# Optimization experiments

Measured on AMD Instinct MI355X. Metric: run time of the kernel, lower is better.

Reference implementation:

```python
import jax, jax.numpy as jnp
import numpy as np

EPS = 1e-5
N_LANG = 5

def _ln(x, gamma, beta):
    mu = jnp.mean(x, axis=-1, keepdims=True)
    var = jnp.mean((x - mu) ** 2, axis=-1, keepdims=True)
    return (x - mu) * jax.lax.rsqrt(var + EPS) * gamma + beta

def setup_inputs() -> dict:
    key = jax.random.key(0)
    ks = jax.random.split(key, 20)
    B, S, E, T, H = 16, 512, 768, 768, 1024
    s = lambda fan_in: 1.0 / np.sqrt(fan_in)
    inp = {
        'ner_features': jax.random.normal(ks[0], (B, S, E), jnp.float32),
        'topic_features': jax.random.normal(ks[1], (B, S, T), jnp.float32),
        'language_ids': jax.random.randint(ks[2], (B,), 0, N_LANG, jnp.int64),
        # ner transform: Linear(E,H) + LayerNorm(H)
        'W_ner': jax.random.uniform(ks[3], (E, H), jnp.float32, -s(E), s(E)),
        'b_ner': jnp.zeros((H,), jnp.float32),
        'g_ner': jnp.ones((H,), jnp.float32),
        'be_ner': jnp.zeros((H,), jnp.float32),
        # topic transform: Linear(T,H) + LayerNorm(H)
        'W_top': jax.random.uniform(ks[4], (T, H), jnp.float32, -s(T), s(T)),
        'b_top': jnp.zeros((H,), jnp.float32),
        'g_top': jnp.ones((H,), jnp.float32),
        'be_top': jnp.zeros((H,), jnp.float32),
        # 5 language gate networks, stacked on leading lang axis
        'Wg1': jax.random.uniform(ks[5], (N_LANG, 2 * H, H), jnp.float32, -s(2 * H), s(2 * H)),
        'bg1': jnp.zeros((N_LANG, H), jnp.float32),
        'gg': jnp.ones((N_LANG, H), jnp.float32),
        'bg': jnp.zeros((N_LANG, H), jnp.float32),
        'Wg2': jax.random.uniform(ks[6], (N_LANG, H, 2), jnp.float32, -s(H), s(H)),
        'bg2': jnp.zeros((N_LANG, 2), jnp.float32),
    }
    return inp

def reference(ner_features, topic_features, language_ids,
              W_ner, b_ner, g_ner, be_ner,
              W_top, b_top, g_top, be_top,
              Wg1, bg1, gg, bg, Wg2, bg2):
    # shared transforms: [B,S,H]
    ner_t = jax.nn.relu(_ln(ner_features @ W_ner + b_ner, g_ner, be_ner))
    top_t = jax.nn.relu(_ln(topic_features @ W_top + b_top, g_top, be_top))
    combined = jnp.concatenate([ner_t, top_t], axis=-1)  # [B,S,2H]
    # all-language gate MLPs (faithful to the original redundant compute)
    h = jnp.einsum('bsd,ldh->lbsh', combined, Wg1) + bg1[:, None, None, :]
    h = jax.nn.relu(_ln(h, gg[:, None, None, :], bg[:, None, None, :]))
    gates_all = jax.nn.sigmoid(jnp.einsum('lbsh,lhk->lbsk', h, Wg2) + bg2[:, None, None, :])  # [L,B,S,2]
    mask = (language_ids[None, :] == jnp.arange(N_LANG)[:, None]).astype(gates_all.dtype)  # [L,B]
    gates = jnp.einsum('lb,lbsk->bsk', mask, gates_all)  # [B,S,2]
    gated_ner = ner_t * gates[..., 0:1]
    gated_topic = top_t * gates[..., 1:2]
    # dropout in eval mode (identity) for determinism
    return gated_ner, gated_topic
```

## Files before the change

kernel.cpp:

```cpp
#include <hip/hip_runtime.h>

typedef __attribute__((ext_vector_type(8))) short short8;
typedef __attribute__((ext_vector_type(4))) float f32x4;

__device__ __forceinline__ float bf2f(unsigned short u) {
    union { unsigned int i; float f; } v; v.i = ((unsigned int)u) << 16; return v.f;
}
__device__ __forceinline__ unsigned short f2bf(float f) {
    union { float f; unsigned int i; } v; v.f = f;
    unsigned int r = v.i + 0x7fffu + ((v.i >> 16) & 1u);
    return (unsigned short)(r >> 16);
}
__device__ __forceinline__ void gload16(const unsigned short* g, unsigned short* l) {
    __builtin_amdgcn_global_load_lds(
        (const __attribute__((address_space(1))) unsigned int*)g,
        (__attribute__((address_space(3))) unsigned int*)l, 16, 0, 0);
}
__device__ __forceinline__ short8 cvt8(float4 a, float4 b) {
    short8 s;
    s[0] = (short)f2bf(a.x); s[1] = (short)f2bf(a.y);
    s[2] = (short)f2bf(a.z); s[3] = (short)f2bf(a.w);
    s[4] = (short)f2bf(b.x); s[5] = (short)f2bf(b.y);
    s[6] = (short)f2bf(b.z); s[7] = (short)f2bf(b.w);
    return s;
}

#define VM(n) asm volatile("s_waitcnt vmcnt(%0)" :: "i"(n) : "memory")
#define LGK0() asm volatile("s_waitcnt lgkmcnt(0)" ::: "memory")
#define SBAR() __builtin_amdgcn_s_barrier()
#define SCHED0() __builtin_amdgcn_sched_barrier(0)

__global__ __launch_bounds__(512, 4) void gemm_f32a(
    const float* __restrict__ nerA, const float* __restrict__ topA,
    const unsigned short* __restrict__ Bta,
    const unsigned short* __restrict__ Btb,
    const float* __restrict__ biasa,
    const float* __restrict__ biasb,
    unsigned short* __restrict__ Cb)
{
    constexpr int K = 768;
    constexpr int NT = K / 64;
    __shared__ __align__(16) unsigned short As0[128][64], Bs0[128][64];
    __shared__ __align__(16) unsigned short As1[128][64], Bs1[128][64];

    const int t = threadIdx.x;
    const int nx = gridDim.x;
    const int bid = blockIdx.y * nx + blockIdx.x;
    const int cpx = (nx * gridDim.y) >> 3;
    const int swz = (bid & 7) * cpx + (bid >> 3);
    const int gm0 = (swz >> 3) * 128;
    const int gn0 = (swz & 7) * 128;

    const int sel = gm0 >> 13;
    const unsigned short* Bt = sel ? Btb : Bta;
    const float* bias = sel ? biasb : biasa;
    const float* Ab = sel ? topA : nerA;

    const int lane = t & 63;
    const int w = t >> 6;
    const int wm = w >> 2, wn = w & 3;
    const int fr = lane & 15, g4 = lane >> 4, f7 = lane & 7;
    const int csw0 = ((0 + g4) ^ f7) * 8;
    const int csw1 = ((4 + g4) ^ f7) * 8;

    const int srow = t >> 3;
    const int swcol = ((t & 7) ^ (srow & 7)) * 8;
    const int lcol = (t & 7) * 8;
    const float* af = Ab + (size_t)((gm0 & 8191) + srow) * K + swcol;
    const unsigned short* bg = Bt + (size_t)(gn0 + srow) * K + swcol;

    f32x4 acc[4][2];
#pragma unroll
    for (int m = 0; m < 4; ++m)
#pragma unroll
        for (int n = 0; n < 2; ++n)
            acc[m][n] = (f32x4){0.f, 0.f, 0.f, 0.f};

    float4 rg0[4], rg1[4];

    auto issueA = [&](float4* rg, int k0) {
        const float4* p0 = (const float4*)(af + k0);
        const float4* p1 = (const float4*)(af + (size_t)64 * K + k0);
        rg[0] = p0[0]; rg[1] = p0[1];
        rg[2] = p1[0]; rg[3] = p1[1];
    };
    auto writeA = [&](unsigned short (*As)[64], const float4* rg) {
        *(short8*)&As[srow][lcol]      = cvt8(rg[0], rg[1]);
        *(short8*)&As[64 + srow][lcol] = cvt8(rg[2], rg[3]);
    };
    auto gloadB = [&](unsigned short (*Bs)[64], int k0) {
#pragma unroll
        for (int i = 0; i < 2; ++i)
            gload16(bg + (size_t)(i * 64) * K + k0, &Bs[i * 64 + srow][lcol]);
    };
    auto compute = [&](const unsigned short (*As)[64], const unsigned short (*Bs)[64]) {
        short8 a0[4], b0[2];
#pragma unroll
        for (int m = 0; m < 4; ++m) a0[m] = *(const short8*)&As[wm * 64 + m * 16 + fr][csw0];
#pragma unroll
        for (int n = 0; n < 2; ++n) b0[n] = *(const short8*)&Bs[wn * 32 + n * 16 + fr][csw0];
        __builtin_amdgcn_s_setprio(1);
#pragma unroll
        for (int m = 0; m < 4; ++m)
#pragma unroll
            for (int n = 0; n < 2; ++n)
                acc[m][n] = __builtin_amdgcn_mfma_f32_16x16x32_bf16(a0[m], b0[n], acc[m][n], 0, 0, 0);
        __builtin_amdgcn_s_setprio(0);
#pragma unroll
        for (int m = 0; m < 4; ++m) a0[m] = *(const short8*)&As[wm * 64 + m * 16 + fr][csw1];
#pragma unroll
        for (int n = 0; n < 2; ++n) b0[n] = *(const short8*)&Bs[wn * 32 + n * 16 + fr][csw1];
        __builtin_amdgcn_s_setprio(1);
#pragma unroll
        for (int m = 0; m < 4; ++m)
#pragma unroll
            for (int n = 0; n < 2; ++n)
                acc[m][n] = __builtin_amdgcn_mfma_f32_16x16x32_bf16(a0[m], b0[n], acc[m][n], 0, 0, 0);
        __builtin_amdgcn_s_setprio(0);
    };

    issueA(rg0, 0);
    gloadB(Bs0, 0);
    issueA(rg1, 64);
    gloadB(Bs1, 64);
    VM(8);
    writeA(As0, rg0);

    for (int tt = 0; tt < NT; tt += 2) {
        if (tt + 1 < NT) VM(2); else VM(0);
        if (tt + 1 < NT) writeA(As1, rg1);
        if (tt + 2 < NT) issueA(rg0, (tt + 2) * 64);
        LGK0();
        SBAR();
        SCHED0();
        compute(As0, Bs0);
        SCHED0();
        SBAR();
        if (tt + 2 < NT) gloadB(Bs0, (tt + 2) * 64);
        if (tt + 2 < NT) VM(2); else VM(0);
        if (tt + 2 < NT) writeA(As0, rg0);
        if (tt + 3 < NT) issueA(rg1, (tt + 3) * 64);
        LGK0();
        SBAR();
        SCHED0();
        compute(As1, Bs1);
        SCHED0();
        SBAR();
        if (tt + 3 < NT) gloadB(Bs1, (tt + 3) * 64);
    }

    const int fq = lane >> 4;
    const int rbase = gm0 & 8191;
    const size_t coloff = (size_t)sel * 1024;
#pragma unroll
    for (int n = 0; n < 2; ++n) {
        const int col = gn0 + wn * 32 + n * 16 + fr;
        const float bv = bias[col];
#pragma unroll
        for (int m = 0; m < 4; ++m) {
            const int row0 = rbase + wm * 64 + m * 16 + fq * 4;
#pragma unroll
            for (int r = 0; r < 4; ++r)
                Cb[(size_t)(row0 + r) * 2048 + coloff + col] = f2bf(acc[m][n][r] + bv);
        }
    }
}

__global__ __launch_bounds__(512, 4) void gemm_w8(
    const unsigned short* __restrict__ A,
    const unsigned short* __restrict__ Bta,
    const float* __restrict__ biasa,
    unsigned short* __restrict__ Cb,
    const int* __restrict__ lang)
{
    constexpr int K = 2048;
    __shared__ __align__(16) unsigned short As0[128][64], Bs0[128][64];
    __shared__ __align__(16) unsigned short As1[128][64], Bs1[128][64];

    const int t = threadIdx.x;
    const int nx = gridDim.x;
    const int bid = blockIdx.y * nx + blockIdx.x;
    const int cpx = (nx * gridDim.y) >> 3;
    const int swz = (bid & 7) * cpx + (bid >> 3);
    const int gm0 = (swz >> 3) * 128;
    const int gn0 = (swz & 7) * 128;

    const int l = lang[gm0 >> 9];
    const unsigned short* Bt = Bta + (size_t)l * ((size_t)K * 1024);
    const float* bias = biasa + l * 1024;

    const int lane = t & 63;
    const int w = t >> 6;
    const int wm = w >> 2, wn = w & 3;
    const int fr = lane & 15, g4 = lane >> 4, f7 = lane & 7;
    const int csw0 = ((0 + g4) ^ f7) * 8;
    const int csw1 = ((4 + g4) ^ f7) * 8;

    const int srow = t >> 3;
    const int swcol = ((t & 7) ^ (srow & 7)) * 8;
    const int lcol = (t & 7) * 8;
    const unsigned short* ag = A  + (size_t)(gm0 + srow) * K + swcol;
    const unsigned short* bg = Bt + (size_t)(gn0 + srow) * K + swcol;

    f32x4 acc[4][2];
#pragma unroll
    for (int m = 0; m < 4; ++m)
#pragma unroll
        for (int n = 0; n < 2; ++n)
            acc[m][n] = (f32x4){0.f, 0.f, 0.f, 0.f};

    auto stage = [&](unsigned short (*As)[64], unsigned short (*Bs)[64], int k0) {
#pragma unroll
        for (int i = 0; i < 2; ++i) {
            gload16(ag + (size_t)(i * 64) * K + k0, &As[i * 64 + srow][lcol]);
            gload16(bg + (size_t)(i * 64) * K + k0, &Bs[i * 64 + srow][lcol]);
        }
    };
    auto compute = [&](const unsigned short (*As)[64], const unsigned short (*Bs)[64]) {
        short8 a0[4], b0[2];
#pragma unroll
        for (int m = 0; m < 4; ++m) a0[m] = *(const short8*)&As[wm * 64 + m * 16 + fr][csw0];
#pragma unroll
        for (int n = 0; n < 2; ++n) b0[n] = *(const short8*)&Bs[wn * 32 + n * 16 + fr][csw0];
        __builtin_amdgcn_s_setprio(1);
#pragma unroll
        for (int m = 0; m < 4; ++m)
#pragma unroll
            for (int n = 0; n < 2; ++n)
                acc[m][n] = __builtin_amdgcn_mfma_f32_16x16x32_bf16(a0[m], b0[n], acc[m][n], 0, 0, 0);
        __builtin_amdgcn_s_setprio(0);
#pragma unroll
        for (int m = 0; m < 4; ++m) a0[m] = *(const short8*)&As[wm * 64 + m * 16 + fr][csw1];
#pragma unroll
        for (int n = 0; n < 2; ++n) b0[n] = *(const short8*)&Bs[wn * 32 + n * 16 + fr][csw1];
        __builtin_amdgcn_s_setprio(1);
#pragma unroll
        for (int m = 0; m < 4; ++m)
#pragma unroll
            for (int n = 0; n < 2; ++n)
                acc[m][n] = __builtin_amdgcn_mfma_f32_16x16x32_bf16(a0[m], b0[n], acc[m][n], 0, 0, 0);
        __builtin_amdgcn_s_setprio(0);
    };

    constexpr int NT = K / 64;
    stage(As0, Bs0, 0);
    stage(As1, Bs1, 64);

    for (int tt = 0; tt < NT; tt += 2) {
        VM(4);
        SBAR();
        asm volatile("" ::: "memory");
        SCHED0();
        compute(As0, Bs0);
        SCHED0();
        SBAR();
        if (tt + 2 < NT) stage(As0, Bs0, (tt + 2) * 64);
        if (tt + 2 < NT) VM(4); else VM(0);
        SBAR();
        asm volatile("" ::: "memory");
        SCHED0();
        compute(As1, Bs1);
        SCHED0();
        SBAR();
        if (tt + 3 < NT) stage(As1, Bs1, (tt + 3) * 64);
    }

    const int fq = lane >> 4;
#pragma unroll
    for (int n = 0; n < 2; ++n) {
        const int col = gn0 + wn * 32 + n * 16 + fr;
        const float bv = bias[col];
#pragma unroll
        for (int m = 0; m < 4; ++m) {
            const int row0 = gm0 + wm * 64 + m * 16 + fq * 4;
#pragma unroll
            for (int r = 0; r < 4; ++r)
                Cb[(size_t)(row0 + r) * 1024 + col] = f2bf(acc[m][n][r] + bv);
        }
    }
}

__device__ __forceinline__ void wt_tile(
    const float* W, unsigned short* Wt, int K, int N, int bx, int by,
    float (*tile)[33], int t)
{
    const int n0 = bx * 32, k0 = by * 32;
    const int x = t & 31, y = t >> 5;
#pragma unroll
    for (int i = 0; i < 4; ++i)
        tile[y + 8 * i][x] = W[(size_t)(k0 + y + 8 * i) * N + n0 + x];
    __syncthreads();
#pragma unroll
    for (int i = 0; i < 4; ++i)
        Wt[(size_t)(n0 + y + 8 * i) * K + k0 + x] = f2bf(tile[x][y + 8 * i]);
}

__global__ __launch_bounds__(256) void prep_all(
    const float* __restrict__ W_ner, unsigned short* __restrict__ W_nert,
    const float* __restrict__ W_top, unsigned short* __restrict__ W_topt,
    const float* __restrict__ Wg1,   unsigned short* __restrict__ Wg1t)
{
    __shared__ float tile[32][33];
    int b = blockIdx.x;
    const int t = threadIdx.x;
    if (b < 768)  { wt_tile(W_ner, W_nert, 768, 1024, b % 32, b / 32, tile, t); return; }
    b -= 768;
    if (b < 768)  { wt_tile(W_top, W_topt, 768, 1024, b % 32, b / 32, tile, t); return; }
    b -= 768;
    const int z = b / 2048, r = b % 2048;
    wt_tile(Wg1 + (size_t)z * 2097152, Wg1t + (size_t)z * 2097152,
            2048, 1024, r % 32, r / 32, tile, t);
}

__global__ __launch_bounds__(256) void ln_relu_c(
    unsigned short* __restrict__ comb,
    const float* __restrict__ gn, const float* __restrict__ bn,
    const float* __restrict__ gt, const float* __restrict__ btp)
{
    const int b = blockIdx.x, t = threadIdx.x;
    const int r = b >> 1, half = b & 1;
    unsigned short* p = comb + (size_t)r * 2048 + half * 1024 + t * 4;
    ushort4 u = *(const ushort4*)p;
    const float x0 = bf2f(u.x), x1 = bf2f(u.y), x2 = bf2f(u.z), x3 = bf2f(u.w);
    float s1 = x0 + x1 + x2 + x3;
    float s2 = x0 * x0 + x1 * x1 + x2 * x2 + x3 * x3;
#pragma unroll
    for (int off = 32; off > 0; off >>= 1) {
        s1 += __shfl_down(s1, off);
        s2 += __shfl_down(s2, off);
    }
    __shared__ float red[8];
    const int wid = t >> 6;
    if ((t & 63) == 0) { red[wid] = s1; red[4 + wid] = s2; }
    __syncthreads();
    s1 = red[0] + red[1] + red[2] + red[3];
    s2 = red[4] + red[5] + red[6] + red[7];
    const float mean = s1 * (1.0f / 1024.0f);
    const float var = fmaxf(s2 * (1.0f / 1024.0f) - mean * mean, 0.0f);
    const float rstd = rsqrtf(var + 1e-5f);
    const float* G  = half ? gt : gn;
    const float* Be = half ? btp : bn;
    const float4 g  = ((const float4*)G)[t];
    const float4 be = ((const float4*)Be)[t];
    u.x = f2bf(fmaxf((x0 - mean) * rstd * g.x + be.x, 0.0f));
    u.y = f2bf(fmaxf((x1 - mean) * rstd * g.y + be.y, 0.0f));
    u.z = f2bf(fmaxf((x2 - mean) * rstd * g.z + be.z, 0.0f));
    u.w = f2bf(fmaxf((x3 - mean) * rstd * g.w + be.w, 0.0f));
    *(ushort4*)p = u;
}

__global__ __launch_bounds__(256) void ln_gate(
    const unsigned short* __restrict__ preln, const unsigned short* __restrict__ comb,
    const float* __restrict__ gg, const float* __restrict__ bgb,
    const float* __restrict__ Wg2, const float* __restrict__ bg2,
    const int* __restrict__ lang,
    float* __restrict__ outN, float* __restrict__ outT)
{
    const int r = blockIdx.x, t = threadIdx.x;
    const int l = lang[r >> 9];
    const ushort4 u = *(const ushort4*)(preln + (size_t)r * 1024 + t * 4);
    const float x0 = bf2f(u.x), x1 = bf2f(u.y), x2 = bf2f(u.z), x3 = bf2f(u.w);
    float s1 = x0 + x1 + x2 + x3;
    float s2 = x0 * x0 + x1 * x1 + x2 * x2 + x3 * x3;
#pragma unroll
    for (int off = 32; off > 0; off >>= 1) {
        s1 += __shfl_down(s1, off);
        s2 += __shfl_down(s2, off);
    }
    __shared__ float red[8];
    const int wid = t >> 6;
    if ((t & 63) == 0) { red[wid] = s1; red[4 + wid] = s2; }
    __syncthreads();
    s1 = red[0] + red[1] + red[2] + red[3];
    s2 = red[4] + red[5] + red[6] + red[7];
    const float mean = s1 * (1.0f / 1024.0f);
    const float var = fmaxf(s2 * (1.0f / 1024.0f) - mean * mean, 0.0f);
    const float rstd = rsqrtf(var + 1e-5f);
    const float4 g  = ((const float4*)(gg + l * 1024))[t];
    const float4 be = ((const float4*)(bgb + l * 1024))[t];
    const float h0 = fmaxf((x0 - mean) * rstd * g.x + be.x, 0.0f);
    const float h1 = fmaxf((x1 - mean) * rstd * g.y + be.y, 0.0f);
    const float h2 = fmaxf((x2 - mean) * rstd * g.z + be.z, 0.0f);
    const float h3 = fmaxf((x3 - mean) * rstd * g.w + be.w, 0.0f);
    const float4* W = (const float4*)(Wg2 + (size_t)l * 2048);
    const float4 wa = W[t * 2], wb = W[t * 2 + 1];
    float d0 = h0 * wa.x + h1 * wa.z + h2 * wb.x + h3 * wb.z;
    float d1 = h0 * wa.y + h1 * wa.w + h2 * wb.y + h3 * wb.w;
#pragma unroll
    for (int off = 32; off > 0; off >>= 1) {
        d0 += __shfl_down(d0, off);
        d1 += __shfl_down(d1, off);
    }
    __syncthreads();
    if ((t & 63) == 0) { red[wid] = d0; red[4 + wid] = d1; }
    __syncthreads();
    d0 = red[0] + red[1] + red[2] + red[3] + bg2[l * 2 + 0];
    d1 = red[4] + red[5] + red[6] + red[7] + bg2[l * 2 + 1];
    const float g0 = 1.0f / (1.0f + __expf(-d0));
    const float g1 = 1.0f / (1.0f + __expf(-d1));
    const ushort4 cn = *(const ushort4*)(comb + (size_t)r * 2048 + t * 4);
    const ushort4 ct = *(const ushort4*)(comb + (size_t)r * 2048 + 1024 + t * 4);
    float4 a, b;
    a.x = bf2f(cn.x) * g0; a.y = bf2f(cn.y) * g0; a.z = bf2f(cn.z) * g0; a.w = bf2f(cn.w) * g0;
    b.x = bf2f(ct.x) * g1; b.y = bf2f(ct.y) * g1; b.z = bf2f(ct.z) * g1; b.w = bf2f(ct.w) * g1;
    ((float4*)(outN + (size_t)r * 1024))[t] = a;
    ((float4*)(outT + (size_t)r * 1024))[t] = b;
}

extern "C" void kernel_launch(void* const* d_in, const int* in_sizes, int n_in,
                              void* d_out, int out_size, void* d_ws, size_t ws_size,
                              hipStream_t stream)
{
    const float* ner    = (const float*)d_in[0];
    const float* top    = (const float*)d_in[1];
    const int*   lang   = (const int*)d_in[2];
    const float* W_ner  = (const float*)d_in[3];
    const float* b_ner  = (const float*)d_in[4];
    const float* g_ner  = (const float*)d_in[5];
    const float* be_ner = (const float*)d_in[6];
    const float* W_top  = (const float*)d_in[7];
    const float* b_top  = (const float*)d_in[8];
    const float* g_top  = (const float*)d_in[9];
    const float* be_top = (const float*)d_in[10];
    const float* Wg1    = (const float*)d_in[11];
    const float* bg1    = (const float*)d_in[12];
    const float* gg     = (const float*)d_in[13];
    const float* bgb    = (const float*)d_in[14];
    const float* Wg2    = (const float*)d_in[15];
    const float* bg2    = (const float*)d_in[16];

    float* out  = (float*)d_out;
    float* outN = out;
    float* outT = out + 8388608;

    char* ws = (char*)d_ws;
    unsigned short* combined = (unsigned short*)ws;
    unsigned short* preln2   = (unsigned short*)(ws + 33554432);
    unsigned short* Wg1t     = (unsigned short*)(ws + 58720256);
    unsigned short* W_nert   = (unsigned short*)outT;
    unsigned short* W_topt   = W_nert + 786432;

    prep_all<<<11776, 256, 0, stream>>>(W_ner, W_nert, W_top, W_topt, Wg1, Wg1t);

    gemm_f32a<<<dim3(8, 128), 512, 0, stream>>>(
        ner, top, W_nert, W_topt, b_ner, b_top, combined);
    ln_relu_c<<<16384, 256, 0, stream>>>(combined, g_ner, be_ner, g_top, be_top);

    gemm_w8<<<dim3(8, 64), 512, 0, stream>>>(combined, Wg1t, bg1, preln2, lang);

    ln_gate<<<8192, 256, 0, stream>>>(preln2, combined, gg, bgb, Wg2, bg2, lang, outN, outT);
}
```

Measured before the change: 138.6 us.

## Pre-convert activations to bf16 and use direct-to-LDS loads with BK=32 in first GEMM

The fp32 ner/topic activations are now converted to bf16 in the prep kernel and stored in workspace. The first GEMM then loads both A and B straight into LDS with global_load_lds, dropping the register staging and in-loop conversion. K-tile depth is halved to 32 to shrink LDS use, and the occupancy hint is raised to 8. The cost is an extra full read and write pass over the activations in the prep kernel, plus twice as many barrier-separated K iterations.

```diff
diff --git a/kernel.cpp b/kernel.cpp
--- a/kernel.cpp
+++ b/kernel.cpp
@@ -16,22 +16,13 @@
         (const __attribute__((address_space(1))) unsigned int*)g,
         (__attribute__((address_space(3))) unsigned int*)l, 16, 0, 0);
 }
-__device__ __forceinline__ short8 cvt8(float4 a, float4 b) {
-    short8 s;
-    s[0] = (short)f2bf(a.x); s[1] = (short)f2bf(a.y);
-    s[2] = (short)f2bf(a.z); s[3] = (short)f2bf(a.w);
-    s[4] = (short)f2bf(b.x); s[5] = (short)f2bf(b.y);
-    s[6] = (short)f2bf(b.z); s[7] = (short)f2bf(b.w);
-    return s;
-}
 
 #define VM(n) asm volatile("s_waitcnt vmcnt(%0)" :: "i"(n) : "memory")
-#define LGK0() asm volatile("s_waitcnt lgkmcnt(0)" ::: "memory")
 #define SBAR() __builtin_amdgcn_s_barrier()
 #define SCHED0() __builtin_amdgcn_sched_barrier(0)
 
-__global__ __launch_bounds__(512, 4) void gemm_f32a(
-    const float* __restrict__ nerA, const float* __restrict__ topA,
+__global__ __launch_bounds__(512, 8) void gemm1_bk32(
+    const unsigned short* __restrict__ A,
     const unsigned short* __restrict__ Bta,
     const unsigned short* __restrict__ Btb,
     const float* __restrict__ biasa,
@@ -39,9 +30,9 @@
     unsigned short* __restrict__ Cb)
 {
     constexpr int K = 768;
-    constexpr int NT = K / 64;
-    __shared__ __align__(16) unsigned short As0[128][64], Bs0[128][64];
-    __shared__ __align__(16) unsigned short As1[128][64], Bs1[128][64];
+    constexpr int NT = K / 32;
+    __shared__ __align__(16) unsigned short As0[128][32], Bs0[128][32];
+    __shared__ __align__(16) unsigned short As1[128][32], Bs1[128][32];
 
     const int t = threadIdx.x;
     const int nx = gridDim.x;
@@ -54,20 +45,17 @@
     const int sel = gm0 >> 13;
     const unsigned short* Bt = sel ? Btb : Bta;
     const float* bias = sel ? biasb : biasa;
-    const float* Ab = sel ? topA : nerA;
 
     const int lane = t & 63;
     const int w = t >> 6;
     const int wm = w >> 2, wn = w & 3;
-    const int fr = lane & 15, g4 = lane >> 4, f7 = lane & 7;
-    const int csw0 = ((0 + g4) ^ f7) * 8;
-    const int csw1 = ((4 + g4) ^ f7) * 8;
-
-    const int srow = t >> 3;
-    const int swcol = ((t & 7) ^ (srow & 7)) * 8;
-    const int lcol = (t & 7) * 8;
-    const float* af = Ab + (size_t)((gm0 & 8191) + srow) * K + swcol;
-    const unsigned short* bg = Bt + (size_t)(gn0 + srow) * K + swcol;
+    const int fr = lane & 15, g4 = lane >> 4;
+    const int csw = (g4 ^ ((fr >> 1) & 3)) * 8;
+
+    const int r = t >> 2, s = t & 3;
+    const int gc = (s ^ ((r >> 1) & 3)) * 8;
+    const unsigned short* ag = A  + (size_t)(gm0 + r) * K + gc;
+    const unsigned short* bg = Bt + (size_t)(gn0 + r) * K + gc;
 
     f32x4 acc[4][2];
 #pragma unroll
@@ -76,40 +64,16 @@
         for (int n = 0; n < 2; ++n)
             acc[m][n] = (f32x4){0.f, 0.f, 0.f, 0.f};
 
-    float4 rg0[4], rg1[4];
-
-    auto issueA = [&](float4* rg, int k0) {
-        const float4* p0 = (const float4*)(af + k0);
-        const float4* p1 = (const float4*)(af + (size_t)64 * K + k0);
-        rg[0] = p0[0]; rg[1] = p0[1];
-        rg[2] = p1[0]; rg[3] = p1[1];
+    auto stage = [&](unsigned short (*As)[32], unsigned short (*Bs)[32], int k0) {
+        gload16(ag + k0, &As[r][s * 8]);
+        gload16(bg + k0, &Bs[r][s * 8]);
     };
-    auto writeA = [&](unsigned short (*As)[64], const float4* rg) {
-        *(short8*)&As[srow][lcol]      = cvt8(rg[0], rg[1]);
-        *(short8*)&As[64 + srow][lcol] = cvt8(rg[2], rg[3]);
-    };
-    auto gloadB = [&](unsigned short (*Bs)[64], int k0) {
-#pragma unroll
-        for (int i = 0; i < 2; ++i)
-            gload16(bg + (size_t)(i * 64) * K + k0, &Bs[i * 64 + srow][lcol]);
-    };
-    auto compute = [&](const unsigned short (*As)[64], const unsigned short (*Bs)[64]) {
+    auto compute = [&](const unsigned short (*As)[32], const unsigned short (*Bs)[32]) {
         short8 a0[4], b0[2];
 #pragma unroll
-        for (int m = 0; m < 4; ++m) a0[m] = *(const short8*)&As[wm * 64 + m * 16 + fr][csw0];
-#pragma unroll
-        for (int n = 0; n < 2; ++n) b0[n] = *(const short8*)&Bs[wn * 32 + n * 16 + fr][csw0];
-        __builtin_amdgcn_s_setprio(1);
-#pragma unroll
-        for (int m = 0; m < 4; ++m)
-#pragma unroll
-            for (int n = 0; n < 2; ++n)
-                acc[m][n] = __builtin_amdgcn_mfma_f32_16x16x32_bf16(a0[m], b0[n], acc[m][n], 0, 0, 0);
-        __builtin_amdgcn_s_setprio(0);
-#pragma unroll
-        for (int m = 0; m < 4; ++m) a0[m] = *(const short8*)&As[wm * 64 + m * 16 + fr][csw1];
-#pragma unroll
-        for (int n = 0; n < 2; ++n) b0[n] = *(const short8*)&Bs[wn * 32 + n * 16 + fr][csw1];
+        for (int m = 0; m < 4; ++m) a0[m] = *(const short8*)&As[wm * 64 + m * 16 + fr][csw];
+#pragma unroll
+        for (int n = 0; n < 2; ++n) b0[n] = *(const short8*)&Bs[wn * 32 + n * 16 + fr][csw];
         __builtin_amdgcn_s_setprio(1);
 #pragma unroll
         for (int m = 0; m < 4; ++m)
@@ -119,34 +83,26 @@
         __builtin_amdgcn_s_setprio(0);
     };
 
-    issueA(rg0, 0);
-    gloadB(Bs0, 0);
-    issueA(rg1, 64);
-    gloadB(Bs1, 64);
-    VM(8);
-    writeA(As0, rg0);
+    stage(As0, Bs0, 0);
+    stage(As1, Bs1, 32);
 
     for (int tt = 0; tt < NT; tt += 2) {
         if (tt + 1 < NT) VM(2); else VM(0);
-        if (tt + 1 < NT) writeA(As1, rg1);
-        if (tt + 2 < NT) issueA(rg0, (tt + 2) * 64);
-        LGK0();
-        SBAR();
+        SBAR();
+        asm volatile("" ::: "memory");
         SCHED0();
         compute(As0, Bs0);
         SCHED0();
         SBAR();
-        if (tt + 2 < NT) gloadB(Bs0, (tt + 2) * 64);
+        if (tt + 2 < NT) stage(As0, Bs0, (tt + 2) * 32);
         if (tt + 2 < NT) VM(2); else VM(0);
-        if (tt + 2 < NT) writeA(As0, rg0);
-        if (tt + 3 < NT) issueA(rg1, (tt + 3) * 64);
-        LGK0();
-        SBAR();
+        SBAR();
+        asm volatile("" ::: "memory");
         SCHED0();
         compute(As1, Bs1);
         SCHED0();
         SBAR();
-        if (tt + 3 < NT) gloadB(Bs1, (tt + 3) * 64);
+        if (tt + 3 < NT) stage(As1, Bs1, (tt + 3) * 32);
     }
 
     const int fq = lane >> 4;
@@ -160,8 +116,8 @@
         for (int m = 0; m < 4; ++m) {
             const int row0 = rbase + wm * 64 + m * 16 + fq * 4;
 #pragma unroll
-            for (int r = 0; r < 4; ++r)
-                Cb[(size_t)(row0 + r) * 2048 + coloff + col] = f2bf(acc[m][n][r] + bv);
+            for (int rr = 0; rr < 4; ++rr)
+                Cb[(size_t)(row0 + rr) * 2048 + coloff + col] = f2bf(acc[m][n][rr] + bv);
         }
     }
 }
@@ -294,11 +250,25 @@
     for (int i = 0; i < 4; ++i)
         Wt[(size_t)(n0 + y + 8 * i) * K + k0 + x] = f2bf(tile[x][y + 8 * i]);
 }
+__device__ __forceinline__ void conv_chunk(
+    const float* in, unsigned short* out, int b, int t)
+{
+    const size_t i = ((size_t)b * 256 + t) * 8;
+    const float4 a = ((const float4*)(in + i))[0];
+    const float4 c = ((const float4*)(in + i))[1];
+    ushort4 u, v;
+    u.x = f2bf(a.x); u.y = f2bf(a.y); u.z = f2bf(a.z); u.w = f2bf(a.w);
+    v.x = f2bf(c.x); v.y = f2bf(c.y); v.z = f2bf(c.z); v.w = f2bf(c.w);
+    *(ushort4*)(out + i)     = u;
+    *(ushort4*)(out + i + 4) = v;
+}
 
 __global__ __launch_bounds__(256) void prep_all(
     const float* __restrict__ W_ner, unsigned short* __restrict__ W_nert,
     const float* __restrict__ W_top, unsigned short* __restrict__ W_topt,
-    const float* __restrict__ Wg1,   unsigned short* __restrict__ Wg1t)
+    const float* __restrict__ Wg1,   unsigned short* __restrict__ Wg1t,
+    const float* __restrict__ ner,   const float* __restrict__ top,
+    unsigned short* __restrict__ actb)
 {
     __shared__ float tile[32][33];
     int b = blockIdx.x;
@@ -307,9 +277,16 @@
     b -= 768;
     if (b < 768)  { wt_tile(W_top, W_topt, 768, 1024, b % 32, b / 32, tile, t); return; }
     b -= 768;
-    const int z = b / 2048, r = b % 2048;
-    wt_tile(Wg1 + (size_t)z * 2097152, Wg1t + (size_t)z * 2097152,
-            2048, 1024, r % 32, r / 32, tile, t);
+    if (b < 10240) {
+        const int z = b / 2048, r = b % 2048;
+        wt_tile(Wg1 + (size_t)z * 2097152, Wg1t + (size_t)z * 2097152,
+                2048, 1024, r % 32, r / 32, tile, t);
+        return;
+    }
+    b -= 10240;
+    if (b < 3072) { conv_chunk(ner, actb, b, t); return; }
+    b -= 3072;
+    conv_chunk(top, actb + 6291456, b, t);
 }
 
 __global__ __launch_bounds__(256) void ln_relu_c(
@@ -435,15 +412,17 @@
 
     char* ws = (char*)d_ws;
     unsigned short* combined = (unsigned short*)ws;
+    unsigned short* actb     = (unsigned short*)(ws + 33554432);
     unsigned short* preln2   = (unsigned short*)(ws + 33554432);
     unsigned short* Wg1t     = (unsigned short*)(ws + 58720256);
     unsigned short* W_nert   = (unsigned short*)outT;
     unsigned short* W_topt   = W_nert + 786432;
 
-    prep_all<<<11776, 256, 0, stream>>>(W_ner, W_nert, W_top, W_topt, Wg1, Wg1t);
-
-    gemm_f32a<<<dim3(8, 128), 512, 0, stream>>>(
-        ner, top, W_nert, W_topt, b_ner, b_top, combined);
+    prep_all<<<17920, 256, 0, stream>>>(W_ner, W_nert, W_top, W_topt,
+                                        Wg1, Wg1t, ner, top, actb);
+
+    gemm1_bk32<<<dim3(8, 128), 512, 0, stream>>>(
+        actb, W_nert, W_topt, b_ner, b_top, combined);
     ln_relu_c<<<16384, 256, 0, stream>>>(combined, g_ner, be_ner, g_top, be_top);
 
     gemm_w8<<<dim3(8, 64), 512, 0, stream>>>(combined, Wg1t, bg1, preln2, lang);
```

New measurement: 159.2 us. 14.8% more time.
